# Kernel optimization log

Hardware: AMD Instinct MI355X
Metric: run time of the kernel (lower is better)

The kernel has to match this reference:

```python
import jax, jax.numpy as jnp
import numpy as np


def setup_inputs() -> dict:
    key = jax.random.key(0)
    k1, k2, k3 = jax.random.split(key, 3)
    B, S_TOT, HD = 2, 4096, 1024
    return {
        "q": jax.random.normal(k1, (B, S_TOT, HD), dtype=jnp.float32),
        "k": jax.random.normal(k2, (B, S_TOT, HD), dtype=jnp.float32),
        "v": jax.random.normal(k3, (B, S_TOT, HD), dtype=jnp.float32),
        "num_heads": 16,
        "num_shots": 4,
        "per_g": 64,
    }


def reference(q, k, v, num_heads, num_shots, per_g):
    # Equal-length shots: shot_latent_indices = [0, L, 2L, ..., s_tot] per batch.
    b, s_tot, hd = q.shape
    d = hd // num_heads
    L = s_tot // num_shots  # local shot length
    scale = 1.0 / jnp.sqrt(jnp.asarray(d, q.dtype))

    # [b, S, L, H, D]
    qs = q.reshape(b, num_shots, L, num_heads, d)
    ks = k.reshape(b, num_shots, L, num_heads, d)
    vs = v.reshape(b, num_shots, L, num_heads, d)

    # Global pool: first per_g tokens of each shot ('firstk'), shared by all shots.
    kg = ks[:, :, :per_g].reshape(b, num_shots * per_g, num_heads, d)  # [b, G, H, D]
    vg = vs[:, :, :per_g].reshape(b, num_shots * per_g, num_heads, d)

    # Block-local scores [b,S,H,L,L] and shared-global scores [b,S,H,L,G]
    s_loc = jnp.einsum("bsqhd,bskhd->bshqk", qs, ks) * scale
    s_glb = jnp.einsum("bsqhd,bghd->bshqg", qs, kg) * scale
    logits = jnp.concatenate([s_loc, s_glb], axis=-1)  # [b,S,H,L,L+G]
    p = jax.nn.softmax(logits, axis=-1)

    o_loc = jnp.einsum("bshqk,bskhd->bsqhd", p[..., :L], vs)
    o_glb = jnp.einsum("bshqg,bghd->bsqhd", p[..., L:], vg)
    out = (o_loc + o_glb).reshape(b, s_tot, hd)
    return out
```

## Files before the change

### kernel.cpp

```cpp
#include <hip/hip_runtime.h>
#include <hip/hip_bf16.h>

#define S_TOT 4096
#define HDIM  1024
#define NH    16
#define DH    64
#define L_    1024
#define NT    19

using bf16x8 = __attribute__((ext_vector_type(8))) short;
using f32x16 = __attribute__((ext_vector_type(16))) float;
using i32x4  = __attribute__((ext_vector_type(4))) int;

typedef const __attribute__((address_space(1))) unsigned int* gp1_t;
typedef __attribute__((address_space(3))) unsigned int* lp3_t;

__device__ __forceinline__ short f2bf(float f) {
    union { float f; unsigned u; } x; x.f = f;
    unsigned r = x.u + 0x7FFFu + ((x.u >> 16) & 1u);
    return (short)(r >> 16);
}

__device__ __forceinline__ unsigned cvt_pk_bf16(float lo, float hi) {
    unsigned r;
    asm("v_cvt_pk_bf16_f32 %0, %1, %2" : "=v"(r) : "v"(lo), "v"(hi));
    return r;
}

__device__ __forceinline__ float exp2_fast(float x) {
#if __has_builtin(__builtin_amdgcn_exp2f)
    return __builtin_amdgcn_exp2f(x);
#else
    return exp2f(x);
#endif
}

__device__ __forceinline__ void gload16(const void* g, void* l) {
    __builtin_amdgcn_global_load_lds((gp1_t)g, (lp3_t)(unsigned long)(l), 16, 0, 0);
}

__global__ __launch_bounds__(256) void prep_kv(
    const float* __restrict__ kf, const float* __restrict__ vf,
    short* __restrict__ kb, short* __restrict__ vb)
{
    __shared__ short st[64 * 70];
    const int bid = blockIdx.x, tid = threadIdx.x;
    if (bid < 1024) {
        const int gid = bid * 256 + tid;
        #pragma unroll
        for (int it = 0; it < 2; ++it) {
            size_t e = ((size_t)gid + (size_t)it * 262144) * 16;
            #pragma unroll
            for (int half = 0; half < 2; ++half) {
                float4 a = *(const float4*)(kf + e + half * 8);
                float4 c = *(const float4*)(kf + e + half * 8 + 4);
                bf16x8 r;
                r[0]=f2bf(a.x); r[1]=f2bf(a.y); r[2]=f2bf(a.z); r[3]=f2bf(a.w);
                r[4]=f2bf(c.x); r[5]=f2bf(c.y); r[6]=f2bf(c.z); r[7]=f2bf(c.w);
                *(bf16x8*)(kb + e + half * 8) = r;
            }
        }
    } else {
        const int vbid = bid - 1024;
        const int stile = vbid & 63, ht = (vbid >> 6) & 15, b = vbid >> 10;
        const int rt = tid >> 2, q4 = tid & 3;
        const float* src = vf + ((size_t)(b * S_TOT + stile * 64 + rt)) * HDIM + ht * 64 + q4 * 16;
        short* dst = st + rt * 70 + q4 * 16;
        #pragma unroll
        for (int i = 0; i < 4; ++i) {
            float4 x = *(const float4*)(src + i * 4);
            dst[i*4+0] = f2bf(x.x); dst[i*4+1] = f2bf(x.y);
            dst[i*4+2] = f2bf(x.z); dst[i*4+3] = f2bf(x.w);
        }
        __syncthreads();
        const int orow = tid >> 2, oq = tid & 3;
        bf16x8 o0, o1;
        #pragma unroll
        for (int j = 0; j < 8; ++j) o0[j] = st[(oq * 16 + j) * 70 + orow];
        #pragma unroll
        for (int j = 0; j < 8; ++j) o1[j] = st[(oq * 16 + 8 + j) * 70 + orow];
        short* dst2 = vb + ((size_t)((b * NH + ht) * 64 + orow)) * S_TOT + stile * 64 + oq * 16;
        *(bf16x8*)dst2 = o0;
        *(bf16x8*)(dst2 + 8) = o1;
    }
}

__global__ __launch_bounds__(256, 2) void attn_kernel(
    const float* __restrict__ qf, const short* __restrict__ kb,
    const short* __restrict__ vb, float* __restrict__ out)
{
    __shared__ __align__(16) char smem[65536];
    const int tid  = threadIdx.x;
    const int wave = tid >> 6, lane = tid & 63;
    const int hi   = lane >> 5, q32 = lane & 31;

    const int bidhw = blockIdx.x;
    const int bid = ((bidhw & 7) << 6) | (bidhw >> 3);
    const int qt = bid & 3, h = (bid >> 2) & 15, s = (bid >> 6) & 3, b = bid >> 8;

    const float CSC = 0.125f * 1.4426950408889634f;
    bf16x8 qv[2][4];
    #pragma unroll
    for (int qs = 0; qs < 2; ++qs) {
        const float* qp = qf + ((size_t)(b*S_TOT + s*L_ + qt*256 + wave*64 + qs*32 + q32)) * HDIM
                             + h * DH + hi * 8;
        #pragma unroll
        for (int d = 0; d < 4; ++d) {
            float4 x0 = *(const float4*)(qp + d * 16);
            float4 x1 = *(const float4*)(qp + d * 16 + 4);
            i32x4 u;
            u[0] = (int)cvt_pk_bf16(x0.x * CSC, x0.y * CSC);
            u[1] = (int)cvt_pk_bf16(x0.z * CSC, x0.w * CSC);
            u[2] = (int)cvt_pk_bf16(x1.x * CSC, x1.y * CSC);
            u[3] = (int)cvt_pk_bf16(x1.z * CSC, x1.w * CSC);
            qv[qs][d] = __builtin_bit_cast(bf16x8, u);
        }
    }

    const int cid = tid, row = cid >> 3;
    const int lch = (cid & 7) ^ (row & 7);
    const int krow = (row & 0x33) | ((row & 4) << 1) | ((row & 8) >> 1);
    const size_t ko = (size_t)krow * 2048 + (lch << 4);
    const size_t vo = (size_t)row  * 8192 + (lch << 4);
    const char* kbase = (const char*)kb + ((size_t)b * S_TOT) * 2048 + h * 128;
    const char* vbase = (const char*)vb + ((size_t)(b * NH + h)) * (64ull * 8192);

    auto abs_tile_of = [&](int t) -> int {
        if (t < 16) return s * 16 + t;
        int g = t - 16; if (g >= s) ++g;
        return g * 16;
    };
    auto stage = [&](int t, int rbase) {
        const int at = abs_tile_of(t);
        const char* kp = kbase + (size_t)at * 131072;
        const char* vp = vbase + (size_t)at * 128;
        char* dst = smem + rbase + wave * 1024;
        gload16(kp + ko,          dst);
        gload16(kp + ko + 65536,  dst + 4096);
        gload16(vp + vo,          dst + 8192);
        gload16(vp + vo + 262144, dst + 12288);
    };

    int qc[4];
    #pragma unroll
    for (int i = 0; i < 4; ++i)
        qc[i] = q32 * 128 + (((i * 2 + hi) ^ (q32 & 7)) << 4);

    f32x16 zro;
    #pragma unroll
    for (int r = 0; r < 16; ++r) zro[r] = 0.f;
    f32x16 acc[2][2];
    acc[0][0] = zro; acc[0][1] = zro; acc[1][0] = zro; acc[1][1] = zro;
    float ps[2] = {0.f, 0.f};

    #define CHUNK(RB, HF, W2) do {                                                 \
        f32x16 S_[2];                                                              \
        {                                                                          \
            __builtin_amdgcn_s_setprio(1);                                         \
            bf16x8 f0 = *(const bf16x8*)(smem + (RB) + (HF)*4096 + qc[0]);         \
            bf16x8 f1 = *(const bf16x8*)(smem + (RB) + (HF)*4096 + qc[1]);         \
            bf16x8 f2 = *(const bf16x8*)(smem + (RB) + (HF)*4096 + qc[2]);         \
            bf16x8 f3 = *(const bf16x8*)(smem + (RB) + (HF)*4096 + qc[3]);         \
            _Pragma("unroll")                                                      \
            for (int qs = 0; qs < 2; ++qs) {                                       \
                f32x16 a = __builtin_amdgcn_mfma_f32_32x32x16_bf16(f0, qv[qs][0], zro, 0,0,0); \
                a = __builtin_amdgcn_mfma_f32_32x32x16_bf16(f1, qv[qs][1], a, 0,0,0); \
                a = __builtin_amdgcn_mfma_f32_32x32x16_bf16(f2, qv[qs][2], a, 0,0,0); \
                a = __builtin_amdgcn_mfma_f32_32x32x16_bf16(f3, qv[qs][3], a, 0,0,0); \
                S_[qs] = a;                                                        \
            }                                                                      \
            __builtin_amdgcn_s_setprio(0);                                         \
        }                                                                          \
        _Pragma("unroll")                                                          \
        for (int qs = 0; qs < 2; ++qs) {                                           \
            _Pragma("unroll")                                                      \
            for (int r = 0; r < 16; ++r)                                           \
                S_[qs][r] = (W2) ? exp2_fast(S_[qs][r] + 1.0f)                     \
                                 : exp2_fast(S_[qs][r]);                           \
            float s0 = (S_[qs][0] + S_[qs][1]) + (S_[qs][2] + S_[qs][3]);          \
            float s1 = (S_[qs][4] + S_[qs][5]) + (S_[qs][6] + S_[qs][7]);          \
            float s2 = (S_[qs][8] + S_[qs][9]) + (S_[qs][10] + S_[qs][11]);        \
            float s3 = (S_[qs][12] + S_[qs][13]) + (S_[qs][14] + S_[qs][15]);      \
            ps[qs] += (s0 + s1) + (s2 + s3);                                       \
        }                                                                          \
        bf16x8 pf0_[2], pf1_[2];                                                   \
        _Pragma("unroll")                                                          \
        for (int qs = 0; qs < 2; ++qs) {                                           \
            i32x4 u;                                                               \
            u[0] = (int)cvt_pk_bf16(S_[qs][0],  S_[qs][1]);                        \
            u[1] = (int)cvt_pk_bf16(S_[qs][2],  S_[qs][3]);                        \
            u[2] = (int)cvt_pk_bf16(S_[qs][4],  S_[qs][5]);                        \
            u[3] = (int)cvt_pk_bf16(S_[qs][6],  S_[qs][7]);                        \
            pf0_[qs] = __builtin_bit_cast(bf16x8, u);                              \
            u[0] = (int)cvt_pk_bf16(S_[qs][8],  S_[qs][9]);                        \
            u[1] = (int)cvt_pk_bf16(S_[qs][10], S_[qs][11]);                       \
            u[2] = (int)cvt_pk_bf16(S_[qs][12], S_[qs][13]);                       \
            u[3] = (int)cvt_pk_bf16(S_[qs][14], S_[qs][15]);                       \
            pf1_[qs] = __builtin_bit_cast(bf16x8, u);                              \
        }                                                                          \
        {                                                                          \
            __builtin_amdgcn_s_setprio(1);                                         \
            bf16x8 w00 = *(const bf16x8*)(smem + (RB) + 8192  + qc[2*(HF)]);       \
            bf16x8 w01 = *(const bf16x8*)(smem + (RB) + 8192  + qc[2*(HF)+1]);     \
            bf16x8 w10 = *(const bf16x8*)(smem + (RB) + 12288 + qc[2*(HF)]);       \
            bf16x8 w11 = *(const bf16x8*)(smem + (RB) + 12288 + qc[2*(HF)+1]);     \
            _Pragma("unroll")                                                      \
            for (int qs = 0; qs < 2; ++qs) {                                       \
                acc[qs][0] = __builtin_amdgcn_mfma_f32_32x32x16_bf16(w00, pf0_[qs], acc[qs][0], 0,0,0); \
                acc[qs][0] = __builtin_amdgcn_mfma_f32_32x32x16_bf16(w01, pf1_[qs], acc[qs][0], 0,0,0); \
                acc[qs][1] = __builtin_amdgcn_mfma_f32_32x32x16_bf16(w10, pf0_[qs], acc[qs][1], 0,0,0); \
                acc[qs][1] = __builtin_amdgcn_mfma_f32_32x32x16_bf16(w11, pf1_[qs], acc[qs][1], 0,0,0); \
            }                                                                      \
            __builtin_amdgcn_s_setprio(0);                                         \
        }                                                                          \
    } while (0)

    #define BARRIER() do {                                                         \
        __builtin_amdgcn_sched_barrier(0);                                         \
        __builtin_amdgcn_s_barrier();                                              \
        __builtin_amdgcn_sched_barrier(0);                                         \
    } while (0)

    stage(0, 0);
    stage(1, 16384);
    asm volatile("s_waitcnt vmcnt(0)" ::: "memory");
    BARRIER();

    stage(2, 32768);
    stage(3, 49152);
    asm volatile("s_waitcnt vmcnt(8)" ::: "memory");
    BARRIER();
    CHUNK(0, 0, 1); CHUNK(0, 1, 1);
    CHUNK(16384, 0, 0); CHUNK(16384, 1, 0);
    BARRIER();

    for (int j = 1; j < 9; ++j) {
        const int rS = (j & 1) ? 0 : 32768;
        const int rC = (j & 1) ? 32768 : 0;
        int ts0 = 2*j + 2, ts1 = 2*j + 3;
        if (ts0 > 18) ts0 = 18;
        if (ts1 > 18) ts1 = 18;
        stage(ts0, rS);
        stage(ts1, rS + 16384);
        asm volatile("s_waitcnt vmcnt(8)" ::: "memory");
        BARRIER();
        CHUNK(rC, 0, 0); CHUNK(rC, 1, 0);
        CHUNK(rC + 16384, 0, 0); CHUNK(rC + 16384, 1, 0);
        BARRIER();
    }

    asm volatile("s_waitcnt vmcnt(0)" ::: "memory");
    BARRIER();
    CHUNK(32768, 0, 0); CHUNK(32768, 1, 0);

    #pragma unroll
    for (int qs = 0; qs < 2; ++qs) {
        float tot = ps[qs] + __shfl_xor(ps[qs], 32);
        float inv = 1.0f / tot;
        const size_t orow = (size_t)(b*S_TOT + s*L_ + qt*256 + wave*64 + qs*32 + q32);
        float* op = out + orow * HDIM + h * DH;
        #pragma unroll
        for (int m = 0; m < 4; ++m) {
            float4 w0, w1;
            w0.x = acc[qs][0][4*m+0]*inv; w0.y = acc[qs][0][4*m+1]*inv;
            w0.z = acc[qs][0][4*m+2]*inv; w0.w = acc[qs][0][4*m+3]*inv;
            *(float4*)(op + 8*m + 4*hi) = w0;
            w1.x = acc[qs][1][4*m+0]*inv; w1.y = acc[qs][1][4*m+1]*inv;
            w1.z = acc[qs][1][4*m+2]*inv; w1.w = acc[qs][1][4*m+3]*inv;
            *(float4*)(op + 32 + 8*m + 4*hi) = w1;
        }
    }
}

extern "C" void kernel_launch(void* const* d_in, const int* in_sizes, int n_in,
                              void* d_out, int out_size, void* d_ws, size_t ws_size,
                              hipStream_t stream) {
    const float* q = (const float*)d_in[0];
    const float* k = (const float*)d_in[1];
    const float* v = (const float*)d_in[2];
    char* ws = (char*)d_ws;
    short* kbuf = (short*)(ws);
    short* vbuf = (short*)(ws + (16u << 20));
    prep_kv<<<dim3(3072), dim3(256), 0, stream>>>(k, v, kbuf, vbuf);
    attn_kernel<<<dim3(512), dim3(256), 0, stream>>>(q, kbuf, vbuf, (float*)d_out);
}
```

Baseline: 75.27 us.

## Halve attention workgroup to two waves and double grid with per-tile double buffer

Shrinks each attention workgroup from 4 waves/256 query rows to 2 waves/128 query rows, doubling the grid to 1024 blocks and halving shared memory to 32KB. The staging pipeline changes from two-tiles-per-stage with four buffers to a single-tile double buffer, with each wave issuing more loads per stage. The aim is more resident blocks per CU and better load balance across the GPU's compute units. The cost is that each K/V tile is now loaded by twice as many workgroups, doubling that traffic, and the prefetch depth is shallower.

```diff
diff --git a/kernel.cpp b/kernel.cpp
--- a/kernel.cpp
+++ b/kernel.cpp
@@ -85,24 +85,24 @@
     }
 }
 
-__global__ __launch_bounds__(256, 2) void attn_kernel(
+__global__ __launch_bounds__(128, 2) void attn_kernel(
     const float* __restrict__ qf, const short* __restrict__ kb,
     const short* __restrict__ vb, float* __restrict__ out)
 {
-    __shared__ __align__(16) char smem[65536];
+    __shared__ __align__(16) char smem[32768];
     const int tid  = threadIdx.x;
     const int wave = tid >> 6, lane = tid & 63;
     const int hi   = lane >> 5, q32 = lane & 31;
 
     const int bidhw = blockIdx.x;
-    const int bid = ((bidhw & 7) << 6) | (bidhw >> 3);
-    const int qt = bid & 3, h = (bid >> 2) & 15, s = (bid >> 6) & 3, b = bid >> 8;
+    const int bid = ((bidhw & 7) << 7) | (bidhw >> 3);
+    const int qt = bid & 7, h = (bid >> 3) & 15, s = (bid >> 7) & 3, b = bid >> 9;
 
     const float CSC = 0.125f * 1.4426950408889634f;
     bf16x8 qv[2][4];
     #pragma unroll
     for (int qs = 0; qs < 2; ++qs) {
-        const float* qp = qf + ((size_t)(b*S_TOT + s*L_ + qt*256 + wave*64 + qs*32 + q32)) * HDIM
+        const float* qp = qf + ((size_t)(b*S_TOT + s*L_ + qt*128 + wave*64 + qs*32 + q32)) * HDIM
                              + h * DH + hi * 8;
         #pragma unroll
         for (int d = 0; d < 4; ++d) {
@@ -117,11 +117,11 @@
         }
     }
 
-    const int cid = tid, row = cid >> 3;
-    const int lch = (cid & 7) ^ (row & 7);
-    const int krow = (row & 0x33) | ((row & 4) << 1) | ((row & 8) >> 1);
-    const size_t ko = (size_t)krow * 2048 + (lch << 4);
-    const size_t vo = (size_t)row  * 8192 + (lch << 4);
+    const int r_low = (wave << 3) | (lane >> 3);
+    const int lch   = (lane & 7) ^ (lane >> 3);
+    const int krow_low = (r_low & 3) | ((r_low & 4) << 1) | ((r_low & 8) >> 1);
+    const size_t ko = (size_t)krow_low * 2048 + (lch << 4);
+    const size_t vo = (size_t)r_low * 8192 + (lch << 4);
     const char* kbase = (const char*)kb + ((size_t)b * S_TOT) * 2048 + h * 128;
     const char* vbase = (const char*)vb + ((size_t)(b * NH + h)) * (64ull * 8192);
 
@@ -130,15 +130,18 @@
         int g = t - 16; if (g >= s) ++g;
         return g * 16;
     };
-    auto stage = [&](int t, int rbase) {
+    auto stage = [&](int t, int bo) {
         const int at = abs_tile_of(t);
         const char* kp = kbase + (size_t)at * 131072;
         const char* vp = vbase + (size_t)at * 128;
-        char* dst = smem + rbase + wave * 1024;
-        gload16(kp + ko,          dst);
-        gload16(kp + ko + 65536,  dst + 4096);
-        gload16(vp + vo,          dst + 8192);
-        gload16(vp + vo + 262144, dst + 12288);
+        char* dK = smem + bo + wave * 1024;
+        char* dV = dK + 8192;
+        #pragma unroll
+        for (int i = 0; i < 4; ++i)
+            gload16(kp + ko + (size_t)i * 32768, dK + i * 2048);
+        #pragma unroll
+        for (int i = 0; i < 4; ++i)
+            gload16(vp + vo + (size_t)i * 131072, dV + i * 2048);
     };
 
     int qc[4];
@@ -153,7 +156,7 @@
     acc[0][0] = zro; acc[0][1] = zro; acc[1][0] = zro; acc[1][1] = zro;
     float ps[2] = {0.f, 0.f};
 
-    #define CHUNK(RB, HF, W2) do {                                                 \
+    #define CHUNK(RB, HF, BIAS) do {                                               \
         f32x16 S_[2];                                                              \
         {                                                                          \
             __builtin_amdgcn_s_setprio(1);                                         \
@@ -175,8 +178,7 @@
         for (int qs = 0; qs < 2; ++qs) {                                           \
             _Pragma("unroll")                                                      \
             for (int r = 0; r < 16; ++r)                                           \
-                S_[qs][r] = (W2) ? exp2_fast(S_[qs][r] + 1.0f)                     \
-                                 : exp2_fast(S_[qs][r]);                           \
+                S_[qs][r] = exp2_fast(S_[qs][r] + (BIAS));                         \
             float s0 = (S_[qs][0] + S_[qs][1]) + (S_[qs][2] + S_[qs][3]);          \
             float s1 = (S_[qs][4] + S_[qs][5]) + (S_[qs][6] + S_[qs][7]);          \
             float s2 = (S_[qs][8] + S_[qs][9]) + (S_[qs][10] + S_[qs][11]);        \
@@ -222,42 +224,30 @@
     } while (0)
 
     stage(0, 0);
-    stage(1, 16384);
     asm volatile("s_waitcnt vmcnt(0)" ::: "memory");
     BARRIER();
 
-    stage(2, 32768);
-    stage(3, 49152);
-    asm volatile("s_waitcnt vmcnt(8)" ::: "memory");
-    BARRIER();
-    CHUNK(0, 0, 1); CHUNK(0, 1, 1);
-    CHUNK(16384, 0, 0); CHUNK(16384, 1, 0);
-    BARRIER();
-
-    for (int j = 1; j < 9; ++j) {
-        const int rS = (j & 1) ? 0 : 32768;
-        const int rC = (j & 1) ? 32768 : 0;
-        int ts0 = 2*j + 2, ts1 = 2*j + 3;
-        if (ts0 > 18) ts0 = 18;
-        if (ts1 > 18) ts1 = 18;
-        stage(ts0, rS);
-        stage(ts1, rS + 16384);
-        asm volatile("s_waitcnt vmcnt(8)" ::: "memory");
+    int bufo = 0;
+    for (int t = 0; t < NT; ++t) {
+        if (t + 1 < NT) {
+            stage(t + 1, bufo ^ 16384);
+            asm volatile("s_waitcnt vmcnt(8)" ::: "memory");
+        } else {
+            asm volatile("s_waitcnt vmcnt(0)" ::: "memory");
+        }
         BARRIER();
-        CHUNK(rC, 0, 0); CHUNK(rC, 1, 0);
-        CHUNK(rC + 16384, 0, 0); CHUNK(rC + 16384, 1, 0);
+        const float bias = (t == 0) ? 1.0f : 0.0f;
+        CHUNK(bufo, 0, bias);
+        CHUNK(bufo, 1, bias);
         BARRIER();
-    }
-
-    asm volatile("s_waitcnt vmcnt(0)" ::: "memory");
-    BARRIER();
-    CHUNK(32768, 0, 0); CHUNK(32768, 1, 0);
+        bufo ^= 16384;
+    }
 
     #pragma unroll
     for (int qs = 0; qs < 2; ++qs) {
         float tot = ps[qs] + __shfl_xor(ps[qs], 32);
         float inv = 1.0f / tot;
-        const size_t orow = (size_t)(b*S_TOT + s*L_ + qt*256 + wave*64 + qs*32 + q32);
+        const size_t orow = (size_t)(b*S_TOT + s*L_ + qt*128 + wave*64 + qs*32 + q32);
         float* op = out + orow * HDIM + h * DH;
         #pragma unroll
         for (int m = 0; m < 4; ++m) {
@@ -282,5 +272,5 @@
     short* kbuf = (short*)(ws);
     short* vbuf = (short*)(ws + (16u << 20));
     prep_kv<<<dim3(3072), dim3(256), 0, stream>>>(k, v, kbuf, vbuf);
-    attn_kernel<<<dim3(512), dim3(256), 0, stream>>>(q, kbuf, vbuf, (float*)d_out);
-}
+    attn_kernel<<<dim3(1024), dim3(128), 0, stream>>>(q, kbuf, vbuf, (float*)d_out);
+}
```

Result: no change. 76.05 us (+1.0%).
